# Performance work log

Measured on AMD Instinct MI355X. Metric: run time of the kernel, lower is better.

The kernel has to match this reference:

```python
import jax, jax.numpy as jnp
import numpy as np
import math

D_MODEL = 1024
N_HEADS = 16
HEAD_DIM = D_MODEL // N_HEADS
THETA = 10000.0


def _rope(x, cos, sin):
    # x: [b, h, s, head_dim]; cos/sin: [s, head_dim//2]
    xe = x[..., 0::2]
    xo = x[..., 1::2]
    re = xe * cos - xo * sin
    ro = xe * sin + xo * cos
    # interleave back to even/odd layout
    return jnp.stack([re, ro], axis=-1).reshape(x.shape)


def setup_inputs() -> dict:
    key = jax.random.key(0)
    k1, k2, k3, k4, k5 = jax.random.split(key, 5)
    std = math.sqrt(2.0 / (D_MODEL + D_MODEL))
    x = jax.random.normal(k1, (2, 2048, D_MODEL), dtype=jnp.float32)
    Wq = jax.random.normal(k2, (D_MODEL, D_MODEL), dtype=jnp.float32) * std
    Wk = jax.random.normal(k3, (D_MODEL, D_MODEL), dtype=jnp.float32) * std
    Wv = jax.random.normal(k4, (D_MODEL, D_MODEL), dtype=jnp.float32) * std
    Wo = jax.random.normal(k5, (D_MODEL, D_MODEL), dtype=jnp.float32) * (std / math.sqrt(2))
    return {"x": x, "Wq": Wq, "Wk": Wk, "Wv": Wv, "Wo": Wo}


def reference(x, Wq, Wk, Wv, Wo):
    b, s, d = x.shape
    h, hd = N_HEADS, HEAD_DIM
    # projections: einsum 'batch seq d_in, d_model d_in -> batch seq d_model' == x @ W.T
    def proj(W):
        y = jnp.einsum('bsd,md->bsm', x, W)
        return y.reshape(b, s, h, hd).transpose(0, 2, 1, 3)  # [b, h, s, hd]
    Q, K, V = proj(Wq), proj(Wk), proj(Wv)
    # RoPE with default positions = arange(seq)
    freqs = 1.0 / (THETA ** (jnp.arange(0, hd, 2, dtype=jnp.float32) / hd))
    angles = jnp.arange(s, dtype=jnp.float32)[:, None] * freqs[None, :]  # [s, hd//2]
    cos, sin = jnp.cos(angles), jnp.sin(angles)
    Q = _rope(Q, cos, sin)
    K = _rope(K, cos, sin)
    # naive causal attention
    scores = jnp.einsum('bhqd,bhkd->bhqk', Q, K) / math.sqrt(hd)
    causal = jnp.tril(jnp.ones((s, s), dtype=bool))
    scores = jnp.where(causal, scores, -jnp.inf)
    attn = jax.nn.softmax(scores, axis=-1)
    out = jnp.einsum('bhqk,bhkd->bhqd', attn, V)
    out = out.transpose(0, 2, 1, 3).reshape(b, s, d)
    return jnp.einsum('bsd,md->bsm', out, Wo)
```

## Files before the change

kernel.cpp:

```cpp
#include <hip/hip_runtime.h>
#include <stdint.h>
#include <stddef.h>

typedef __bf16 bf16;
typedef __bf16 bf16x8 __attribute__((ext_vector_type(8)));
typedef __bf16 bf16x4 __attribute__((ext_vector_type(4)));
typedef short short4v __attribute__((ext_vector_type(4)));
typedef float f32x4 __attribute__((ext_vector_type(4)));

#define GAS __attribute__((address_space(1)))
#define LAS __attribute__((address_space(3)))

__device__ __forceinline__ void async_load16(const void* g, void* l) {
  __builtin_amdgcn_global_load_lds((const GAS void*)g, (LAS void*)l, 16, 0, 0);
}

__device__ __forceinline__ f32x4 mfma16(bf16x4 a, bf16x4 b, f32x4 c) {
#if defined(__HIP_DEVICE_COMPILE__)
#if __has_builtin(__builtin_amdgcn_mfma_f32_16x16x16bf16_1k)
  return __builtin_amdgcn_mfma_f32_16x16x16bf16_1k(
      __builtin_bit_cast(short4v, a), __builtin_bit_cast(short4v, b), c, 0, 0, 0);
#else
  f32x4 d;
  asm volatile("v_mfma_f32_16x16x16_bf16 %0, %1, %2, %3"
               : "=v"(d)
               : "v"(a), "v"(b), "v"(c));
  return d;
#endif
#else
  (void)a; (void)b;
  return c;
#endif
}

__global__ __launch_bounds__(256) void cast_all(
    const float* __restrict__ x, const float* __restrict__ Wq,
    const float* __restrict__ Wk, const float* __restrict__ Wv,
    const float* __restrict__ Wo, bf16* __restrict__ Xh,
    bf16* __restrict__ Wqkv, bf16* __restrict__ Woh,
    float2* __restrict__ rope) {
  if (blockIdx.x >= 8192) {
    const int e = ((blockIdx.x - 8192) * 256 + threadIdx.x) * 4;
    const int s = e >> 5, ip0 = e & 31;
#pragma unroll
    for (int r = 0; r < 4; ++r) {
      const float freq = __expf((float)(ip0 + r) * -0.2878231366242557f);
      float sn, cs;
      __sincosf((float)s * freq, &sn, &cs);
      rope[e + r] = make_float2(cs, sn);
    }
    return;
  }
  int idx = (blockIdx.x * 256 + threadIdx.x) * 4;
  const float* src;
  bf16* dst;
  float scale = 1.0f;
  if (idx < 4194304) {
    src = x + idx; dst = Xh + idx;
  } else if (idx < 7340032) {
    int j = idx - 4194304;
    if (j < 1048576) {
      src = Wq + j; scale = 0.18033688011112042f;
    } else {
      src = ((j < 2097152) ? Wk : Wv) + (j & 1048575);
    }
    dst = Wqkv + j;
  } else {
    int j = idx - 7340032;
    src = Wo + j; dst = Woh + j;
  }
  float4 v = *(const float4*)src;
  bf16x4 o;
  o[0] = (bf16)(v.x * scale); o[1] = (bf16)(v.y * scale);
  o[2] = (bf16)(v.z * scale); o[3] = (bf16)(v.w * scale);
  *(bf16x4*)dst = o;
}

__global__ __launch_bounds__(256, 3) void gemm_qkv(
    const bf16* __restrict__ A, const bf16* __restrict__ B,
    const float2* __restrict__ rope, bf16* __restrict__ Qh,
    bf16* __restrict__ Kh, bf16* __restrict__ Vt, int K) {
  __shared__ __align__(16) bf16 As[128 * 64];
  __shared__ __align__(16) bf16 Bs[128 * 64];
  const int tid = threadIdx.x;
  const int wave = tid >> 6, lane = tid & 63;
  const int bm = blockIdx.y * 128, bn = blockIdx.x * 128;
  const int wm = (wave >> 1) * 64, wn = (wave & 1) * 64;
  const int fr = lane & 15, g = lane >> 4;
  const int sw8 = (fr & 7) * 8;

  const int srow = tid >> 3;
  const int scol = 8 * ((tid & 7) ^ (srow & 7));
  const int ldst = wave * 512;

  f32x4 acc[4][4] = {};

  for (int kt = 0; kt < K; kt += 64) {
    __syncthreads();
#pragma unroll
    for (int s = 0; s < 4; ++s) {
      const int row = s * 32 + srow;
      async_load16(A + (size_t)(bm + row) * K + kt + scol,
                   (void*)(As + s * 2048 + ldst));
      async_load16(B + (size_t)(bn + row) * K + kt + scol,
                   (void*)(Bs + s * 2048 + ldst));
    }
    __syncthreads();

#pragma unroll
    for (int ks = 0; ks < 2; ++ks) {
      bf16x8 af[4], bfr[4];
      const int kq = (ks * 32 + g * 8) ^ sw8;
#pragma unroll
      for (int i = 0; i < 4; ++i)
        af[i] = *(const bf16x8*)&As[(wm + i * 16 + fr) * 64 + kq];
#pragma unroll
      for (int j = 0; j < 4; ++j)
        bfr[j] = *(const bf16x8*)&Bs[(wn + j * 16 + fr) * 64 + kq];
#pragma unroll
      for (int i = 0; i < 4; ++i)
#pragma unroll
        for (int j = 0; j < 4; ++j)
          acc[i][j] = __builtin_amdgcn_mfma_f32_16x16x32_bf16(af[i], bfr[j],
                                                              acc[i][j], 0, 0, 0);
    }
  }

  const int r0 = (lane >> 4) * 4, cc = lane & 15;
  const bool oddl = cc & 1;
#pragma unroll
  for (int i = 0; i < 4; ++i) {
    const int row0 = bm + wm + i * 16 + r0;
    const int b = row0 >> 11, s0 = row0 & 2047;
#pragma unroll
    for (int j = 0; j < 4; ++j) {
      const int col = bn + wn + j * 16 + cc;
      if (col < 2048) {
        const int hcol = col & 1023;
        const int h = hcol >> 6, d = hcol & 63;
        const int ip = d >> 1;
        const bool isK = col >= 1024;
        bf16* dst = (isK ? Kh : Qh) + ((size_t)(b * 16 + h) * 2048) * 64;
#pragma unroll
        for (int r = 0; r < 4; ++r) {
          float own = acc[i][j][r];
          float oth = __shfl_xor(own, 1, 64);
          const float2 t = rope[((s0 + r) << 5) + ip];
          float res = oddl ? (oth * t.y + own * t.x) : (own * t.x - oth * t.y);
          const int dd = isK ? (d ^ (((s0 + r) & 7) << 3)) : d;
          dst[(size_t)(s0 + r) * 64 + dd] = (bf16)res;
        }
      } else {
        const int v = col - 2048, h = v >> 6, d = v & 63;
        bf16x4 o;
#pragma unroll
        for (int r = 0; r < 4; ++r) o[r] = (bf16)acc[i][j][r];
        const int s2 = (s0 & ~63) | ((s0 ^ ((d & 7) << 3)) & 63);
        *(bf16x4*)&Vt[(((size_t)b * 16 + h) * 64 + d) * 2048 + s2] = o;
      }
    }
  }
}

template <typename OutT, int BM, int BN>
__global__ __launch_bounds__(256) void gemm_bt(
    const bf16* __restrict__ A, const bf16* __restrict__ B,
    OutT* __restrict__ C, int M, int N, int K) {
  constexpr int ACH = BM / 16, NCH = (BM + BN) / 16, PW = NCH / 4;
  constexpr int FM = BM / 32, FN = BN / 32;
  __shared__ __align__(16) bf16 As[BM * 32];
  __shared__ __align__(16) bf16 Bs[BN * 32];
  const int tid = threadIdx.x;
  const int wave = tid >> 6, lane = tid & 63;
  const int bm = blockIdx.y * BM, bn = blockIdx.x * BN;
  const int wm = (wave >> 1) * (BM / 2), wn = (wave & 1) * (BN / 2);
  const int lrow = lane >> 2, lk = (lane & 3) * 8;
  const int fr = lane & 15, fk = (lane >> 4) * 8;

  f32x4 acc[FM][FN] = {};

  for (int kt = 0; kt < K; kt += 32) {
    __syncthreads();
#pragma unroll
    for (int c = 0; c < PW; ++c) {
      const int chunk = wave * PW + c;
      if (chunk < ACH) {
        const bf16* ga = A + (size_t)(bm + chunk * 16 + lrow) * K + kt + lk;
        async_load16(ga, (void*)(As + chunk * 512));
      } else {
        const int bc = chunk - ACH;
        const bf16* gb = B + (size_t)(bn + bc * 16 + lrow) * K + kt + lk;
        async_load16(gb, (void*)(Bs + bc * 512));
      }
    }
    __syncthreads();

    bf16x8 af[FM], bfr[FN];
#pragma unroll
    for (int i = 0; i < FM; ++i)
      af[i] = *(const bf16x8*)&As[(wm + i * 16 + fr) * 32 + fk];
#pragma unroll
    for (int j = 0; j < FN; ++j)
      bfr[j] = *(const bf16x8*)&Bs[(wn + j * 16 + fr) * 32 + fk];
#pragma unroll
    for (int i = 0; i < FM; ++i)
#pragma unroll
      for (int j = 0; j < FN; ++j)
        acc[i][j] =
            __builtin_amdgcn_mfma_f32_16x16x32_bf16(af[i], bfr[j], acc[i][j], 0, 0, 0);
  }

  const int r0 = (lane >> 4) * 4, cc = lane & 15;
#pragma unroll
  for (int i = 0; i < FM; ++i)
#pragma unroll
    for (int j = 0; j < FN; ++j)
#pragma unroll
      for (int r = 0; r < 4; ++r)
        C[(size_t)(bm + wm + i * 16 + r0 + r) * N + (bn + wn + j * 16 + cc)] =
            (OutT)acc[i][j][r];
}

__global__ __launch_bounds__(256, 2) void attn(const bf16* __restrict__ Qh,
                                               const bf16* __restrict__ Kh,
                                               const bf16* __restrict__ Vt,
                                               bf16* __restrict__ Oh) {
  __shared__ __align__(16) bf16 Ks[3][64 * 64];
  __shared__ __align__(16) bf16 Vs[3][64 * 64];
  const int f = blockIdx.x;
  int j, bh;
  if (f < 256) { bh = f >> 4;              j = 15 - (f & 15); }
  else         { bh = 16 + ((f - 256) >> 4); j = f & 15; }
  const int tid = threadIdx.x, w = tid >> 6, lane = tid & 63;
  const int nlo = lane & 15, g = lane >> 4;
  const int q0 = j * 128, qw0 = q0 + w * 32;
  const bf16* __restrict__ Qp = Qh + (size_t)bh * 131072;
  const bf16* __restrict__ Kp = Kh + (size_t)bh * 131072;
  const bf16* __restrict__ Vp = Vt + (size_t)bh * 131072;
  const int n = 2 * (j + 1);
  const int nw = 2 * j + (w >> 1) + 1;

  bf16x8 aq[2][2];
#pragma unroll
  for (int qb = 0; qb < 2; ++qb)
#pragma unroll
    for (int ks = 0; ks < 2; ++ks)
      aq[qb][ks] =
          *(const bf16x8*)&Qp[(size_t)(qw0 + qb * 16 + nlo) * 64 + ks * 32 + g * 8];

  f32x4 oacc[2][4] = {};
  float lsum[2] = {0.f, 0.f};
  const int sw = (nlo & 7) << 3;

  const int srow = w * 16 + (lane >> 3);
  const int soff = (lane & 7) * 8;

  auto stage = [&](int slot, int kbase) {
    async_load16(Kp + (size_t)(kbase + srow) * 64 + soff,
                 (void*)(Ks[slot] + w * 1024));
    async_load16(Kp + (size_t)(kbase + srow + 8) * 64 + soff,
                 (void*)(Ks[slot] + w * 1024 + 512));
    async_load16(Vp + (size_t)srow * 2048 + kbase + soff,
                 (void*)(Vs[slot] + w * 1024));
    async_load16(Vp + (size_t)(srow + 8) * 2048 + kbase + soff,
                 (void*)(Vs[slot] + w * 1024 + 512));
  };

  bf16x8 pk[4][2];
  auto rdK = [&](int slot) {
    const bf16* __restrict__ Kw = Ks[slot];
#pragma unroll
    for (int ni = 0; ni < 4; ++ni)
#pragma unroll
      for (int ks = 0; ks < 2; ++ks)
        pk[ni][ks] =
            *(const bf16x8*)&Kw[(ni * 16 + nlo) * 64 + ((ks * 32 + g * 8) ^ sw)];
  };

  bf16x4 av[4][4];
  auto rdV = [&](int slot) {
    const bf16* __restrict__ Vw = Vs[slot];
#pragma unroll
    for (int ni = 0; ni < 4; ++ni)
#pragma unroll
      for (int mi = 0; mi < 4; ++mi)
        av[ni][mi] =
            *(const bf16x4*)&Vw[(mi * 16 + nlo) * 64 + ((ni * 16 + g * 4) ^ sw)];
  };

  f32x4 st[2][4];
  auto qk = [&]() {
#pragma unroll
    for (int qb = 0; qb < 2; ++qb) {
#pragma unroll
      for (int ni = 0; ni < 4; ++ni) st[qb][ni] = f32x4{0.f, 0.f, 0.f, 0.f};
#pragma unroll
      for (int ks = 0; ks < 2; ++ks)
#pragma unroll
        for (int ni = 0; ni < 4; ++ni)
          st[qb][ni] = __builtin_amdgcn_mfma_f32_16x16x32_bf16(
              pk[ni][ks], aq[qb][ks], st[qb][ni], 0, 0, 0);
    }
  };

  bf16x4 p[2][4];
  auto expv = [&](int i) {
    const int kbase = i * 64;
    const bool dg = (i == nw - 1);
#pragma unroll
    for (int qb = 0; qb < 2; ++qb) {
      const int qg = qw0 + qb * 16 + nlo;
      if (!dg) {
#pragma unroll
        for (int ni = 0; ni < 4; ++ni)
#pragma unroll
          for (int r = 0; r < 4; ++r) {
            float e = __builtin_amdgcn_exp2f(st[qb][ni][r]);
            lsum[qb] += e;
            p[qb][ni][r] = (bf16)e;
          }
      } else {
#pragma unroll
        for (int ni = 0; ni < 4; ++ni) {
          const int kg0 = kbase + ni * 16 + g * 4;
#pragma unroll
          for (int r = 0; r < 4; ++r) {
            float e = __builtin_amdgcn_exp2f(st[qb][ni][r]);
            e = (kg0 + r <= qg) ? e : 0.0f;
            lsum[qb] += e;
            p[qb][ni][r] = (bf16)e;
          }
        }
      }
    }
  };

  auto pv = [&]() {
#pragma unroll
    for (int ni = 0; ni < 4; ++ni)
#pragma unroll
      for (int mi = 0; mi < 4; ++mi)
#pragma unroll
        for (int qb = 0; qb < 2; ++qb)
          oacc[qb][mi] = mfma16(av[ni][mi], p[qb][ni], oacc[qb][mi]);
  };

  stage(0, 0);
  stage(1, 64);
  __syncthreads();
  rdK(0);
  qk();
  expv(0);

  for (int i = 0; i < n - 1; ++i) {
    const int i1 = i + 1;
    if (i + 2 < n) stage((i + 2) % 3, (i + 2) * 64);
    const bool doQK = (i1 < nw);
    if (doQK) rdK(i1 % 3);
    rdV(i % 3);
    __builtin_amdgcn_s_setprio(1);
    if (doQK) qk();
    pv();
    __builtin_amdgcn_s_setprio(0);
    if (doQK) expv(i1);
    __syncthreads();
  }

  if (nw == n) {
    rdV((n - 1) % 3);
    pv();
  }

#pragma unroll
  for (int qb = 0; qb < 2; ++qb) {
    lsum[qb] += __shfl_xor(lsum[qb], 16, 64);
    lsum[qb] += __shfl_xor(lsum[qb], 32, 64);
  }

  const int bb = bh >> 4, hd = bh & 15;
#pragma unroll
  for (int qb = 0; qb < 2; ++qb) {
    const float inv = 1.0f / lsum[qb];
    const int q = qw0 + qb * 16 + nlo;
#pragma unroll
    for (int mi = 0; mi < 4; ++mi) {
      bf16x4 o;
#pragma unroll
      for (int r = 0; r < 4; ++r) o[r] = (bf16)(oacc[qb][mi][r] * inv);
      *(bf16x4*)&Oh[((size_t)bb * 2048 + q) * 1024 + hd * 64 + mi * 16 + g * 4] = o;
    }
  }
}

extern "C" void kernel_launch(void* const* d_in, const int* in_sizes, int n_in,
                              void* d_out, int out_size, void* d_ws, size_t ws_size,
                              hipStream_t stream) {
  (void)in_sizes; (void)n_in; (void)out_size; (void)ws_size;
  const float* x = (const float*)d_in[0];
  const float* Wq = (const float*)d_in[1];
  const float* Wk = (const float*)d_in[2];
  const float* Wv = (const float*)d_in[3];
  const float* Wo = (const float*)d_in[4];
  float* out = (float*)d_out;
  char* ws = (char*)d_ws;

  bf16* Xh    = (bf16*)(ws);
  bf16* Wqkv  = (bf16*)(ws + 8388608);
  bf16* Woh   = (bf16*)(ws + 14680064);
  bf16* Qh    = (bf16*)(ws + 16777216);
  bf16* Kh    = (bf16*)(ws + 25165824);
  bf16* Vt    = (bf16*)(ws + 33554432);
  bf16* Oh    = (bf16*)(ws + 41943040);
  float2* rope = (float2*)(ws + 50331648);

  cast_all<<<8256, 256, 0, stream>>>(x, Wq, Wk, Wv, Wo, Xh, Wqkv, Woh, rope);
  gemm_qkv<<<dim3(24, 32), 256, 0, stream>>>(Xh, Wqkv, rope, Qh, Kh, Vt, 1024);
  attn<<<512, 256, 0, stream>>>(Qh, Kh, Vt, Oh);
  gemm_bt<float, 128, 128><<<dim3(8, 32), 256, 0, stream>>>(Oh, Woh, out, 4096, 1024, 1024);
}
```

Baseline: 178.1 us.

## Deepen GEMM K-tile with swizzled LDS and relax attention pipeline waits

The projection GEMM now stages 64-wide K tiles instead of 32, using an XOR-swizzled LDS layout to avoid bank conflicts. This halves the number of barrier-separated iterations. The attention kernel maps blocks so that heads group by XCD, adds a fourth V buffer, and replaces full __syncthreads with partial vmcnt waits plus s_barrier, so loads for later tiles can stay in flight. The cost is more LDS and hand-written waitcnt logic that relies on an exact count of outstanding loads.

Result: slower. 182.9 us, median of 2 (+2.7%).

```diff
diff --git a/kernel.cpp b/kernel.cpp
--- a/kernel.cpp
+++ b/kernel.cpp
@@ -166,48 +166,51 @@
 __global__ __launch_bounds__(256) void gemm_bt(
     const bf16* __restrict__ A, const bf16* __restrict__ B,
     OutT* __restrict__ C, int M, int N, int K) {
-  constexpr int ACH = BM / 16, NCH = (BM + BN) / 16, PW = NCH / 4;
   constexpr int FM = BM / 32, FN = BN / 32;
-  __shared__ __align__(16) bf16 As[BM * 32];
-  __shared__ __align__(16) bf16 Bs[BN * 32];
+  constexpr int SA = BM / 32, SB = BN / 32;
+  __shared__ __align__(16) bf16 As[BM * 64];
+  __shared__ __align__(16) bf16 Bs[BN * 64];
   const int tid = threadIdx.x;
   const int wave = tid >> 6, lane = tid & 63;
   const int bm = blockIdx.y * BM, bn = blockIdx.x * BN;
   const int wm = (wave >> 1) * (BM / 2), wn = (wave & 1) * (BN / 2);
-  const int lrow = lane >> 2, lk = (lane & 3) * 8;
-  const int fr = lane & 15, fk = (lane >> 4) * 8;
+  const int fr = lane & 15, g = lane >> 4;
+  const int sw8 = (fr & 7) * 8;
+  const int srow = tid >> 3;
+  const int scol = 8 * ((tid & 7) ^ (srow & 7));
+  const int ldst = wave * 512;
 
   f32x4 acc[FM][FN] = {};
 
-  for (int kt = 0; kt < K; kt += 32) {
+  for (int kt = 0; kt < K; kt += 64) {
     __syncthreads();
 #pragma unroll
-    for (int c = 0; c < PW; ++c) {
-      const int chunk = wave * PW + c;
-      if (chunk < ACH) {
-        const bf16* ga = A + (size_t)(bm + chunk * 16 + lrow) * K + kt + lk;
-        async_load16(ga, (void*)(As + chunk * 512));
-      } else {
-        const int bc = chunk - ACH;
-        const bf16* gb = B + (size_t)(bn + bc * 16 + lrow) * K + kt + lk;
-        async_load16(gb, (void*)(Bs + bc * 512));
-      }
-    }
+    for (int s = 0; s < SA; ++s)
+      async_load16(A + (size_t)(bm + s * 32 + srow) * K + kt + scol,
+                   (void*)(As + s * 2048 + ldst));
+#pragma unroll
+    for (int s = 0; s < SB; ++s)
+      async_load16(B + (size_t)(bn + s * 32 + srow) * K + kt + scol,
+                   (void*)(Bs + s * 2048 + ldst));
     __syncthreads();
 
-    bf16x8 af[FM], bfr[FN];
-#pragma unroll
-    for (int i = 0; i < FM; ++i)
-      af[i] = *(const bf16x8*)&As[(wm + i * 16 + fr) * 32 + fk];
-#pragma unroll
-    for (int j = 0; j < FN; ++j)
-      bfr[j] = *(const bf16x8*)&Bs[(wn + j * 16 + fr) * 32 + fk];
-#pragma unroll
-    for (int i = 0; i < FM; ++i)
+#pragma unroll
+    for (int ks = 0; ks < 2; ++ks) {
+      const int kq = (ks * 32 + g * 8) ^ sw8;
+      bf16x8 af[FM], bfr[FN];
+#pragma unroll
+      for (int i = 0; i < FM; ++i)
+        af[i] = *(const bf16x8*)&As[(wm + i * 16 + fr) * 64 + kq];
 #pragma unroll
       for (int j = 0; j < FN; ++j)
-        acc[i][j] =
-            __builtin_amdgcn_mfma_f32_16x16x32_bf16(af[i], bfr[j], acc[i][j], 0, 0, 0);
+        bfr[j] = *(const bf16x8*)&Bs[(wn + j * 16 + fr) * 64 + kq];
+#pragma unroll
+      for (int i = 0; i < FM; ++i)
+#pragma unroll
+        for (int j = 0; j < FN; ++j)
+          acc[i][j] = __builtin_amdgcn_mfma_f32_16x16x32_bf16(af[i], bfr[j],
+                                                              acc[i][j], 0, 0, 0);
+    }
   }
 
   const int r0 = (lane >> 4) * 4, cc = lane & 15;
@@ -226,11 +229,11 @@
                                                const bf16* __restrict__ Vt,
                                                bf16* __restrict__ Oh) {
   __shared__ __align__(16) bf16 Ks[3][64 * 64];
-  __shared__ __align__(16) bf16 Vs[3][64 * 64];
+  __shared__ __align__(16) bf16 Vs[4][64 * 64];
   const int f = blockIdx.x;
-  int j, bh;
-  if (f < 256) { bh = f >> 4;              j = 15 - (f & 15); }
-  else         { bh = 16 + ((f - 256) >> 4); j = f & 15; }
+  const int xcd = f & 7, u = (f >> 3) & 31, v = f >> 8;
+  const int bh = xcd + 8 * (u & 3);
+  const int j = v ? (u >> 2) : 15 - (u >> 2);
   const int tid = threadIdx.x, w = tid >> 6, lane = tid & 63;
   const int nlo = lane & 15, g = lane >> 4;
   const int q0 = j * 128, qw0 = q0 + w * 32;
@@ -255,15 +258,16 @@
   const int srow = w * 16 + (lane >> 3);
   const int soff = (lane & 7) * 8;
 
-  auto stage = [&](int slot, int kbase) {
+  auto stage = [&](int i) {
+    const int kbase = i * 64, sk = i % 3, sv = i & 3;
     async_load16(Kp + (size_t)(kbase + srow) * 64 + soff,
-                 (void*)(Ks[slot] + w * 1024));
+                 (void*)(Ks[sk] + w * 1024));
     async_load16(Kp + (size_t)(kbase + srow + 8) * 64 + soff,
-                 (void*)(Ks[slot] + w * 1024 + 512));
+                 (void*)(Ks[sk] + w * 1024 + 512));
     async_load16(Vp + (size_t)srow * 2048 + kbase + soff,
-                 (void*)(Vs[slot] + w * 1024));
+                 (void*)(Vs[sv] + w * 1024));
     async_load16(Vp + (size_t)(srow + 8) * 2048 + kbase + soff,
-                 (void*)(Vs[slot] + w * 1024 + 512));
+                 (void*)(Vs[sv] + w * 1024 + 512));
   };
 
   bf16x8 pk[4][2];
@@ -345,29 +349,31 @@
           oacc[qb][mi] = mfma16(av[ni][mi], p[qb][ni], oacc[qb][mi]);
   };
 
-  stage(0, 0);
-  stage(1, 64);
-  __syncthreads();
-  rdK(0);
-  qk();
-  expv(0);
-
-  for (int i = 0; i < n - 1; ++i) {
-    const int i1 = i + 1;
-    if (i + 2 < n) stage((i + 2) % 3, (i + 2) * 64);
-    const bool doQK = (i1 < nw);
-    if (doQK) rdK(i1 % 3);
-    rdV(i % 3);
+  stage(0);
+  stage(1);
+  asm volatile("s_waitcnt vmcnt(4)" ::: "memory");
+  __builtin_amdgcn_s_barrier();
+
+  for (int i = 0; i < n; ++i) {
+    if (i + 2 < n) stage(i + 2);
+    const bool doQK = (i < nw);
+    const bool doPV = (i > 0);
+    if (doQK) rdK(i % 3);
+    if (doPV) rdV((i - 1) & 3);
     __builtin_amdgcn_s_setprio(1);
     if (doQK) qk();
-    pv();
+    if (doPV) pv();
     __builtin_amdgcn_s_setprio(0);
-    if (doQK) expv(i1);
-    __syncthreads();
+    if (doQK) expv(i);
+    if (i + 2 < n)
+      asm volatile("s_waitcnt vmcnt(4)" ::: "memory");
+    else
+      asm volatile("s_waitcnt vmcnt(0)" ::: "memory");
+    __builtin_amdgcn_s_barrier();
   }
 
   if (nw == n) {
-    rdV((n - 1) % 3);
+    rdV((n - 1) & 3);
     pv();
   }
 
```
